# Kernel tuning notes

Hardware: AMD Instinct MI355X
Metric: run time of the kernel (lower is better)

Reference implementation:

```python
import jax, jax.numpy as jnp
import numpy as np
from jax import lax

B, C, H, W = 16, 1, 1024, 1024
BOUNDARY_WEIGHT = 3.0
# two iterations of a flat 5x5 structuring element == one flat 9x9 window
WIN = 9
PAD = WIN // 2


def setup_inputs() -> dict:
    key = jax.random.key(0)
    k1, k2, k3, k4 = jax.random.split(key, 4)
    logits = jax.random.normal(k1, (B, C, H, W), dtype=jnp.float32)
    # spatially-coherent binary masks (random disks), mimicking car masks
    cy = jax.random.uniform(k2, (B,), minval=0.3 * H, maxval=0.7 * H)
    cx = jax.random.uniform(k3, (B,), minval=0.3 * W, maxval=0.7 * W)
    r = jax.random.uniform(k4, (B,), minval=0.15 * H, maxval=0.4 * H)
    ys = jnp.arange(H, dtype=jnp.float32)
    xs = jnp.arange(W, dtype=jnp.float32)
    d2 = (ys[None, :, None] - cy[:, None, None]) ** 2 + (xs[None, None, :] - cx[:, None, None]) ** 2
    targets = (d2 < (r[:, None, None] ** 2)).astype(jnp.float32)[:, None]  # [B,1,H,W]
    return {"logits": logits, "targets": targets}


def _morph(t, op, init):
    # flat-SE morphology over HxW via reduce_window; cv2 default border is
    # the neutral value for the op, matching init padding.
    return lax.reduce_window(
        t, init, op,
        window_dimensions=(1, 1, WIN, WIN),
        window_strides=(1, 1, 1, 1),
        padding=[(0, 0), (0, 0), (PAD, PAD), (PAD, PAD)],
    )


def reference(logits, targets):
    dilated = _morph(targets, lax.max, -jnp.inf)
    eroded = _morph(targets, lax.min, jnp.inf)
    boundary = dilated - eroded  # 1 on mask boundary band, else 0
    weights = 1.0 + (BOUNDARY_WEIGHT - 1.0) * boundary
    # stable BCE-with-logits: max(x,0) - x*y + log1p(exp(-|x|))
    x, y = logits, targets
    per_elem = jnp.maximum(x, 0.0) - x * y + jax.nn.softplus(-jnp.abs(x))
    return jnp.mean(weights * per_elem)
```

## Files before the change

### kernel.cpp

```cpp
#include <hip/hip_runtime.h>

#define BATCH 16
#define IMG_H 1024
#define IMG_W 1024
#define WORDS 16
#define TY 32
#define SROWS (TY + 8)
#define NT 512
#define NWAVES (NT / 64)

typedef unsigned long long u64;

__global__ void wbce_zero_kernel(float* out) { out[0] = 0.0f; }

__global__ __launch_bounds__(NT, 4)
void wbce_kernel(const float* __restrict__ logits,
                 const float* __restrict__ targets,
                 float* __restrict__ out)
{
    __shared__ u64 sT [SROWS * WORDS];
    __shared__ u64 sHD[SROWS * WORDS];
    __shared__ u64 sHE[SROWS * WORDS];
    __shared__ u64 sBnd[TY * WORDS];
    __shared__ float sRed[NWAVES];

    const int tid  = threadIdx.x;
    const int lane = tid & 63;
    const int wv   = tid >> 6;
    const int rowBase = blockIdx.x * TY;
    const int b = blockIdx.y;

    const float* tgt = targets + (size_t)b * (IMG_H * IMG_W);
    const float* lg  = logits  + (size_t)b * (IMG_H * IMG_W);

    for (int it4 = wv * 4; it4 < SROWS * WORDS; it4 += NWAVES * 4) {
        int sr = it4 >> 4;
        int gr = rowBase + sr - 4;
        float v0 = 0.f, v1 = 0.f, v2 = 0.f, v3 = 0.f;
        if (gr >= 0 && gr < IMG_H) {
            const float* rp = tgt + (size_t)gr * IMG_W + ((it4 & 15) * 64) + lane;
            v0 = rp[0]; v1 = rp[64]; v2 = rp[128]; v3 = rp[192];
        }
        u64 m0 = __ballot(v0 > 0.5f);
        u64 m1 = __ballot(v1 > 0.5f);
        u64 m2 = __ballot(v2 > 0.5f);
        u64 m3 = __ballot(v3 > 0.5f);
        if (lane == 0) {
            sT[it4]     = m0; sT[it4 + 1] = m1;
            sT[it4 + 2] = m2; sT[it4 + 3] = m3;
        }
    }
    __syncthreads();

    for (int it = tid; it < SROWS * WORDS; it += NT) {
        int sr = it >> 4;
        int w  = it & 15;
        int gr = rowBase + sr - 4;
        u64 hd = 0ULL, he = ~0ULL;
        if (gr >= 0 && gr < IMG_H) {
            u64 C  = sT[it];
            u64 P  = (w > 0)  ? sT[it - 1] : 0ULL;
            u64 N  = (w < 15) ? sT[it + 1] : 0ULL;
            u64 Pe = (w > 0)  ? P : ~0ULL;
            u64 Ne = (w < 15) ? N : ~0ULL;
            u64 d = C, e = C;
            #pragma unroll
            for (int s = 1; s <= 4; ++s) {
                d |= (C >> s) | (N  << (64 - s));
                d |= (C << s) | (P  >> (64 - s));
                e &= (C >> s) | (Ne << (64 - s));
                e &= (C << s) | (Pe >> (64 - s));
            }
            hd = d; he = e;
        }
        sHD[it] = hd;
        sHE[it] = he;
    }
    __syncthreads();

    {
        int r = tid >> 4, w = tid & 15;
        u64 d = 0ULL, e = ~0ULL;
        #pragma unroll
        for (int k = 0; k < 9; ++k) {
            d |= sHD[(r + k) * WORDS + w];
            e &= sHE[(r + k) * WORDS + w];
        }
        sBnd[tid] = d & ~e;
    }
    __syncthreads();

    const float4* base = (const float4*)(lg + (size_t)rowBase * IMG_W);
    const unsigned* sBnd32 = (const unsigned*)sBnd;
    const unsigned* sT32   = (const unsigned*)sT;

    float acc = 0.0f;
    float4 bufA[4], bufB[4];
    #pragma unroll
    for (int j = 0; j < 4; ++j) bufA[j] = base[tid + j * NT];

    #pragma unroll
    for (int kb = 0; kb < 4; ++kb) {
        float4* cur = (kb & 1) ? bufB : bufA;
        float4* nxt = (kb & 1) ? bufA : bufB;
        if (kb < 3) {
            #pragma unroll
            for (int j = 0; j < 4; ++j)
                nxt[j] = base[tid + ((kb + 1) * 4 + j) * NT];
        }
        #pragma unroll
        for (int j = 0; j < 4; ++j) {
            int it  = tid + (kb * 4 + j) * NT;
            int r   = it >> 8;
            int pos = it & 255;
            int wi  = r * WORDS + (pos >> 4);
            int hf  = (pos >> 3) & 1;
            int sh  = (pos & 7) * 4;
            unsigned bbw = sBnd32[wi * 2 + hf];
            unsigned tbw = sT32[(wi + 4 * WORDS) * 2 + hf];

            const float xs[4] = {cur[j].x, cur[j].y, cur[j].z, cur[j].w};
            #pragma unroll
            for (int jj = 0; jj < 4; ++jj) {
                unsigned tb = (tbw >> (sh + jj)) & 1u;
                unsigned bb = (bbw >> (sh + jj)) & 1u;
                unsigned xu = __float_as_uint(xs[jj]);
                float sgn = __uint_as_float(xu ^ (tb << 31));
                float a   = __uint_as_float(xu & 0x7fffffffu);
                float t   = __builtin_exp2f(a * -1.44269504088896340736f);
                float l2  = __builtin_log2f(1.0f + t);
                float pe  = fmaf(l2, 0.69314718055994530942f, fmaxf(sgn, 0.0f));
                float wg  = fmaf((float)bb, 2.0f, 1.0f);
                acc = fmaf(wg, pe, acc);
            }
        }
    }

    #pragma unroll
    for (int off = 32; off > 0; off >>= 1)
        acc += __shfl_down(acc, off, 64);
    if (lane == 0) sRed[wv] = acc;
    __syncthreads();
    if (tid == 0) {
        float s = 0.0f;
        #pragma unroll
        for (int i = 0; i < NWAVES; ++i) s += sRed[i];
        atomicAdd(out, s * (1.0f / 16777216.0f));
    }
}

extern "C" void kernel_launch(void* const* d_in, const int* in_sizes, int n_in,
                              void* d_out, int out_size, void* d_ws, size_t ws_size,
                              hipStream_t stream) {
    const float* logits  = (const float*)d_in[0];
    const float* targets = (const float*)d_in[1];
    float* out = (float*)d_out;

    wbce_zero_kernel<<<dim3(1), dim3(1), 0, stream>>>(out);

    dim3 grid(IMG_H / TY, BATCH);
    dim3 block(NT);
    wbce_kernel<<<grid, block, 0, stream>>>(logits, targets, out);
}
```

Before: 37.50 us.

## Prefetch logits with inline asm loads before the morphology phase

Half of each thread's logits tile is now loaded with inline-asm global_load_dwordx4 at kernel start, so those reads overlap the target bitmask and dilation/erosion phases. The other half is issued after the morphology phase and waited on with an explicit s_waitcnt before it is consumed. The logits-to-thread mapping changes so each wave owns four contiguous rows. The compiler cannot track the asm loads, so correctness depends on the barriers and waitcnts it inserts elsewhere. The early loads also compete with the target reads and keep more live registers.

```diff
diff --git a/kernel.cpp b/kernel.cpp
--- a/kernel.cpp
+++ b/kernel.cpp
@@ -10,6 +10,7 @@
 #define NWAVES (NT / 64)
 
 typedef unsigned long long u64;
+typedef float f32x4 __attribute__((ext_vector_type(4)));
 
 __global__ void wbce_zero_kernel(float* out) { out[0] = 0.0f; }
 
@@ -32,6 +33,22 @@
 
     const float* tgt = targets + (size_t)b * (IMG_H * IMG_W);
     const float* lg  = logits  + (size_t)b * (IMG_H * IMG_W);
+
+    const float* a0 = lg + (size_t)rowBase * IMG_W + (wv << 12) + (lane << 2);
+    const float* a1 = a0 + 1024;
+    f32x4 p0, p1, p2, p3, p4, p5, p6, p7;
+    asm volatile(
+        "global_load_dwordx4 %0, %8, off\n\t"
+        "global_load_dwordx4 %1, %8, off offset:1024\n\t"
+        "global_load_dwordx4 %2, %8, off offset:2048\n\t"
+        "global_load_dwordx4 %3, %8, off offset:3072\n\t"
+        "global_load_dwordx4 %4, %9, off\n\t"
+        "global_load_dwordx4 %5, %9, off offset:1024\n\t"
+        "global_load_dwordx4 %6, %9, off offset:2048\n\t"
+        "global_load_dwordx4 %7, %9, off offset:3072"
+        : "=&v"(p0), "=&v"(p1), "=&v"(p2), "=&v"(p3),
+          "=&v"(p4), "=&v"(p5), "=&v"(p6), "=&v"(p7)
+        : "v"(a0), "v"(a1));
 
     for (int it4 = wv * 4; it4 < SROWS * WORDS; it4 += NWAVES * 4) {
         int sr = it4 >> 4;
@@ -90,51 +107,61 @@
     }
     __syncthreads();
 
-    const float4* base = (const float4*)(lg + (size_t)rowBase * IMG_W);
+    const float* a2 = a0 + 2048;
+    const float* a3 = a0 + 3072;
+    f32x4 q0, q1, q2, q3, q4, q5, q6, q7;
+    asm volatile(
+        "global_load_dwordx4 %0, %8, off\n\t"
+        "global_load_dwordx4 %1, %8, off offset:1024\n\t"
+        "global_load_dwordx4 %2, %8, off offset:2048\n\t"
+        "global_load_dwordx4 %3, %8, off offset:3072\n\t"
+        "global_load_dwordx4 %4, %9, off\n\t"
+        "global_load_dwordx4 %5, %9, off offset:1024\n\t"
+        "global_load_dwordx4 %6, %9, off offset:2048\n\t"
+        "global_load_dwordx4 %7, %9, off offset:3072"
+        : "=&v"(q0), "=&v"(q1), "=&v"(q2), "=&v"(q3),
+          "=&v"(q4), "=&v"(q5), "=&v"(q6), "=&v"(q7)
+        : "v"(a2), "v"(a3));
+
     const unsigned* sBnd32 = (const unsigned*)sBnd;
     const unsigned* sT32   = (const unsigned*)sT;
+    float acc = 0.0f;
 
-    float acc = 0.0f;
-    float4 bufA[4], bufB[4];
-    #pragma unroll
-    for (int j = 0; j < 4; ++j) bufA[j] = base[tid + j * NT];
+    #define CONSUME(x4, m)                                                    \
+    do {                                                                      \
+        int idx = (m) * 64 + lane;             \
+        int r   = (wv << 2) + (idx >> 8);                \
+        int pos = idx & 255;                           \
+        int wi  = r * WORDS + (pos >> 4);                                     \
+        int hf  = (pos >> 3) & 1;                                             \
+        int sh  = (pos & 7) * 4;                                              \
+        unsigned bbw = sBnd32[wi * 2 + hf];                                   \
+        unsigned tbw = sT32[(wi + 4 * WORDS) * 2 + hf];          \
+        const float xs[4] = {x4.x, x4.y, x4.z, x4.w};                         \
+        _Pragma("unroll")                                                     \
+        for (int jj = 0; jj < 4; ++jj) {                                      \
+            unsigned tb = (tbw >> (sh + jj)) & 1u;                            \
+            unsigned bb = (bbw >> (sh + jj)) & 1u;                            \
+            unsigned xu = __float_as_uint(xs[jj]);                            \
+            float sgn = __uint_as_float(xu ^ (tb << 31));                     \
+            float av  = __uint_as_float(xu & 0x7fffffffu);                    \
+            float t   = __builtin_exp2f(av * -1.44269504088896340736f);       \
+            float l2  = __builtin_log2f(1.0f + t);                            \
+            float pe  = fmaf(l2, 0.69314718055994530942f, fmaxf(sgn, 0.0f));  \
+            float wg  = fmaf((float)bb, 2.0f, 1.0f);   \
+            acc = fmaf(wg, pe, acc);                                          \
+        }                                                                     \
+    } while (0)
 
-    #pragma unroll
-    for (int kb = 0; kb < 4; ++kb) {
-        float4* cur = (kb & 1) ? bufB : bufA;
-        float4* nxt = (kb & 1) ? bufA : bufB;
-        if (kb < 3) {
-            #pragma unroll
-            for (int j = 0; j < 4; ++j)
-                nxt[j] = base[tid + ((kb + 1) * 4 + j) * NT];
-        }
-        #pragma unroll
-        for (int j = 0; j < 4; ++j) {
-            int it  = tid + (kb * 4 + j) * NT;
-            int r   = it >> 8;
-            int pos = it & 255;
-            int wi  = r * WORDS + (pos >> 4);
-            int hf  = (pos >> 3) & 1;
-            int sh  = (pos & 7) * 4;
-            unsigned bbw = sBnd32[wi * 2 + hf];
-            unsigned tbw = sT32[(wi + 4 * WORDS) * 2 + hf];
+    CONSUME(p0, 0); CONSUME(p1, 1); CONSUME(p2, 2); CONSUME(p3, 3);
+    CONSUME(p4, 4); CONSUME(p5, 5); CONSUME(p6, 6); CONSUME(p7, 7);
 
-            const float xs[4] = {cur[j].x, cur[j].y, cur[j].z, cur[j].w};
-            #pragma unroll
-            for (int jj = 0; jj < 4; ++jj) {
-                unsigned tb = (tbw >> (sh + jj)) & 1u;
-                unsigned bb = (bbw >> (sh + jj)) & 1u;
-                unsigned xu = __float_as_uint(xs[jj]);
-                float sgn = __uint_as_float(xu ^ (tb << 31));
-                float a   = __uint_as_float(xu & 0x7fffffffu);
-                float t   = __builtin_exp2f(a * -1.44269504088896340736f);
-                float l2  = __builtin_log2f(1.0f + t);
-                float pe  = fmaf(l2, 0.69314718055994530942f, fmaxf(sgn, 0.0f));
-                float wg  = fmaf((float)bb, 2.0f, 1.0f);
-                acc = fmaf(wg, pe, acc);
-            }
-        }
-    }
+    asm volatile("s_waitcnt vmcnt(0)"
+        : "+v"(q0), "+v"(q1), "+v"(q2), "+v"(q3),
+          "+v"(q4), "+v"(q5), "+v"(q6), "+v"(q7));
+    CONSUME(q0, 8);  CONSUME(q1, 9);  CONSUME(q2, 10); CONSUME(q3, 11);
+    CONSUME(q4, 12); CONSUME(q5, 13); CONSUME(q6, 14); CONSUME(q7, 15);
+    #undef CONSUME
 
     #pragma unroll
     for (int off = 32; off > 0; off >>= 1)
```

Result: slower. 41.05 us (+9.4%).
